# Optimization experiments

Hardware: AMD Instinct MI355X
Metric: run time of the kernel (lower is better)

Reference implementation:

```python
import jax, jax.numpy as jnp
import numpy as np

TOP_K = 2

def setup_inputs() -> dict:
    key = jax.random.key(0)
    k0, k1, k2, k3, k4 = jax.random.split(key, 5)
    B, S, D, H, E = 2, 2048, 1024, 2048, 8
    x = jax.random.normal(k0, (B, S, D), dtype=jnp.float32)
    router_w = jax.random.normal(k1, (D, E), dtype=jnp.float32) * (1.0 / np.sqrt(D))
    wg = jax.random.normal(k2, (E, D, H), dtype=jnp.float32) * (1.0 / np.sqrt(D))
    wu = jax.random.normal(k3, (E, D, H), dtype=jnp.float32) * (1.0 / np.sqrt(D))
    wd = jax.random.normal(k4, (E, H, D), dtype=jnp.float32) * (1.0 / np.sqrt(H))
    return {"x": x, "router_w": router_w, "wg": wg, "wu": wu, "wd": wd}

def reference(x, router_w, wg, wu, wd):
    B, S, D = x.shape
    E = router_w.shape[1]
    xf = x.reshape(-1, D)                                   # [T, D]
    router_logits = xf @ router_w                           # [T, E]
    top_logits, top_idx = jax.lax.top_k(router_logits, TOP_K)
    top_w = jax.nn.softmax(top_logits, axis=-1)             # [T, k]
    # Dense combine weights: W[t, e] = routing weight if e in top-k of t, else 0.
    combine = jnp.sum(jax.nn.one_hot(top_idx, E, dtype=x.dtype) * top_w[..., None], axis=1)  # [T, E]
    # SwiGLU experts, computed for all tokens and masked by the combine weights
    # (mathematically identical to the gather/scatter form in the original).
    gate = jnp.einsum('td,edh->eth', xf, wg)                # [E, T, H]
    up = jnp.einsum('td,edh->eth', xf, wu)                  # [E, T, H]
    fused = jax.nn.silu(gate) * up                          # [E, T, H]
    expert_out = jnp.einsum('eth,ehd->etd', fused, wd)      # [E, T, D]
    y = jnp.einsum('etd,te->td', expert_out, combine)       # [T, D]
    return y.reshape(B, S, D)
```

## Files before the change

kernel.cpp:

```cpp
#include <hip/hip_runtime.h>
#include <hip/hip_bf16.h>

#define T_TOK 4096
#define DDIM  1024
#define HDIM  2048
#define NEXP  8
#define BK 64

typedef __attribute__((ext_vector_type(4))) float f32x4;
typedef __attribute__((ext_vector_type(8))) short s16x8;
typedef __hip_bfloat16 bf16;

typedef const void __attribute__((address_space(1))) gvoid;
typedef void __attribute__((address_space(3))) svoid;

__device__ __forceinline__ void gload16(const void* g, void* l) {
    __builtin_amdgcn_global_load_lds((gvoid*)g, (svoid*)l, 16, 0, 0);
}

__global__ void router_kernel(const float* __restrict__ x, const float* __restrict__ rw,
                              int* __restrict__ r_e, float* __restrict__ r_w) {
    int wave = threadIdx.x >> 6, lane = threadIdx.x & 63;
    int t = blockIdx.x * 4 + wave;
    if (t >= T_TOK) return;
    const float* xr = x + (size_t)t * DDIM;
    double acc[NEXP];
#pragma unroll
    for (int e = 0; e < NEXP; ++e) acc[e] = 0.0;
    for (int d = lane; d < DDIM; d += 64) {
        float xv = xr[d];
        const float* rwr = rw + (size_t)d * NEXP;
#pragma unroll
        for (int e = 0; e < NEXP; ++e) acc[e] += (double)xv * (double)rwr[e];
    }
#pragma unroll
    for (int e = 0; e < NEXP; ++e) {
#pragma unroll
        for (int off = 32; off > 0; off >>= 1) acc[e] += __shfl_down(acc[e], off);
    }
    if (lane == 0) {
        int i0 = 0; double v0 = acc[0];
#pragma unroll
        for (int e = 1; e < NEXP; ++e) if (acc[e] > v0) { v0 = acc[e]; i0 = e; }
        int i1 = -1; double v1 = -1e300;
#pragma unroll
        for (int e = 0; e < NEXP; ++e) { if (e == i0) continue; if (acc[e] > v1) { v1 = acc[e]; i1 = e; } }
        float w0 = 1.0f / (1.0f + expf((float)(v1 - v0)));
        float w1 = 1.0f - w0;
        r_e[2*t]   = i0; r_e[2*t+1] = i1;
        r_w[2*t]   = w0; r_w[2*t+1] = w1;
    }
}

__global__ void count_kernel(const int* __restrict__ r_e, int* __restrict__ cnt) {
    int i = blockIdx.x * blockDim.x + threadIdx.x;
    if (i < 2 * T_TOK) atomicAdd(&cnt[r_e[i]], 1);
}
__global__ void scan_kernel(const int* __restrict__ cnt, int* __restrict__ offs) {
    if (threadIdx.x == 0) {
        int s = 0;
        for (int e = 0; e < NEXP; ++e) { offs[e] = s; s += cnt[e]; }
        offs[NEXP] = s;
    }
}
__global__ void fill_kernel(const int* __restrict__ r_e, const int* __restrict__ offs,
                            int* __restrict__ cnt2, const float* __restrict__ r_w,
                            int* __restrict__ list, float* __restrict__ slot_w) {
    int i = blockIdx.x * blockDim.x + threadIdx.x;
    if (i < 2 * T_TOK) {
        int e = r_e[i];
        int pos = atomicAdd(&cnt2[e], 1);
        int slot = offs[e] + pos;
        list[slot] = i >> 1;
        slot_w[slot] = r_w[i];
    }
}

__global__ void transpose_cast_kernel(const float* __restrict__ in, bf16* __restrict__ out,
                                      int R, int C, int rmul, int roff, size_t outE) {
    __shared__ bf16 tile[64][68];
    const float* inp = in + (size_t)blockIdx.z * R * C;
    bf16* outp = out + (size_t)blockIdx.z * outE;
    int r0 = blockIdx.x * 64, c0 = blockIdx.y * 64;
    int tid = threadIdx.x;
#pragma unroll
    for (int i = 0; i < 4; ++i) {
        int idx = i * 256 + tid;
        int r = idx >> 4, c4 = (idx & 15) * 4;
        float4 v = *reinterpret_cast<const float4*>(inp + (size_t)(r0 + r) * C + c0 + c4);
        tile[r][c4 + 0] = __float2bfloat16(v.x);
        tile[r][c4 + 1] = __float2bfloat16(v.y);
        tile[r][c4 + 2] = __float2bfloat16(v.z);
        tile[r][c4 + 3] = __float2bfloat16(v.w);
    }
    __syncthreads();
#pragma unroll
    for (int i = 0; i < 4; ++i) {
        int idx = i * 256 + tid;
        int c = idx >> 4, r4 = (idx & 15) * 4;
        union { ushort4 u; bf16 h[4]; } w;
        w.h[0] = tile[r4 + 0][c];
        w.h[1] = tile[r4 + 1][c];
        w.h[2] = tile[r4 + 2][c];
        w.h[3] = tile[r4 + 3][c];
        *reinterpret_cast<ushort4*>(outp + ((size_t)(c0 + c) * rmul + roff) * R + r0 + r4) = w.u;
    }
}

__global__ void cast_x_kernel(const float* __restrict__ x, bf16* __restrict__ xb) {
    size_t i = (size_t)(blockIdx.x * blockDim.x + threadIdx.x) * 4;
    float4 v = *reinterpret_cast<const float4*>(x + i);
    union { ushort4 u; bf16 h[4]; } o;
    o.h[0] = __float2bfloat16(v.x);
    o.h[1] = __float2bfloat16(v.y);
    o.h[2] = __float2bfloat16(v.z);
    o.h[3] = __float2bfloat16(v.w);
    *reinterpret_cast<ushort4*>(xb + i) = o.u;
}

__global__ __launch_bounds__(512, 4)
void gateup_kernel(const bf16* __restrict__ xb, const bf16* __restrict__ wguT,
                   const int* __restrict__ offs, const int* __restrict__ list,
                   bf16* __restrict__ hbuf) {
    int e = blockIdx.z;
    int base = offs[e];
    int ne = offs[e + 1] - base;
    int m0 = blockIdx.y * 128;
    if (m0 >= ne) return;
    int n0 = blockIdx.x * 128;

    __shared__ bf16 As[2][128 * 64];
    __shared__ bf16 Bs[2][128 * 64];

    int tid = threadIdx.x, lane = tid & 63, wid = tid >> 6;
    int sub = lane >> 3;
    int swz = 8 * ((lane & 7) ^ sub);

    const bf16* bbase = wguT + (size_t)e * (2 * HDIM) * DDIM + (size_t)n0 * DDIM;

    const bf16* aS[2]; const bf16* bS[2];
#pragma unroll
    for (int i = 0; i < 2; ++i) {
        int row = i * 64 + wid * 8 + sub;
        int r = m0 + row; if (r > ne - 1) r = ne - 1;
        aS[i] = xb + (size_t)list[base + r] * DDIM + swz;
        bS[i] = bbase + (size_t)row * DDIM + swz;
    }
    int dst0 = (wid * 8) * 64, dst1 = (64 + wid * 8) * 64;

    int wrow = (wid >> 2) * 64;
    int wcol = (wid & 3) * 32;
    int rl = lane & 15, kq = 8 * (lane >> 4);
    int xorv = (rl & 7) * 8;

    f32x4 zero4 = {0.f, 0.f, 0.f, 0.f};
    f32x4 acc[4][2];
#pragma unroll
    for (int mi = 0; mi < 4; ++mi) { acc[mi][0] = zero4; acc[mi][1] = zero4; }

    const int nk = DDIM / BK;

    gload16(aS[0], &As[0][dst0]);
    gload16(aS[1], &As[0][dst1]);
    gload16(bS[0], &Bs[0][dst0]);
    gload16(bS[1], &Bs[0][dst1]);
    gload16(aS[0] + BK, &As[1][dst0]);
    gload16(aS[1] + BK, &As[1][dst1]);
    gload16(bS[0] + BK, &Bs[1][dst0]);
    gload16(bS[1] + BK, &Bs[1][dst1]);

#define GU_COMPUTE(Ab, Bb)                                                        \
    _Pragma("unroll")                                                             \
    for (int kk = 0; kk < 2; ++kk) {                                              \
        int kos = (kk * 32 + kq) ^ xorv;                                          \
        s16x8 a[4], b[2];                                                         \
        _Pragma("unroll")                                                         \
        for (int mi = 0; mi < 4; ++mi)                                            \
            a[mi] = *reinterpret_cast<const s16x8*>(&(Ab)[(wrow + mi * 16 + rl) * 64 + kos]); \
        _Pragma("unroll")                                                         \
        for (int ni = 0; ni < 2; ++ni)                                            \
            b[ni] = *reinterpret_cast<const s16x8*>(&(Bb)[(wcol + ni * 16 + rl) * 64 + kos]); \
        _Pragma("unroll")                                                         \
        for (int mi = 0; mi < 4; ++mi)                                            \
            _Pragma("unroll")                                                     \
            for (int ni = 0; ni < 2; ++ni)                                        \
                acc[mi][ni] = __builtin_amdgcn_mfma_f32_16x16x32_bf16(a[mi], b[ni], acc[mi][ni], 0, 0, 0); \
    }

    for (int t = 0; t < nk - 1; ++t) {
        asm volatile("s_waitcnt vmcnt(4)" ::: "memory");
        __builtin_amdgcn_s_barrier();
        GU_COMPUTE(As[t & 1], Bs[t & 1]);
        __builtin_amdgcn_sched_barrier(0);
        __builtin_amdgcn_s_barrier();
        if (t + 2 < nk) {
            int k0 = (t + 2) * BK;
            gload16(aS[0] + k0, &As[t & 1][dst0]);
            gload16(aS[1] + k0, &As[t & 1][dst1]);
            gload16(bS[0] + k0, &Bs[t & 1][dst0]);
            gload16(bS[1] + k0, &Bs[t & 1][dst1]);
        }
    }
    asm volatile("s_waitcnt vmcnt(0)" ::: "memory");
    __builtin_amdgcn_s_barrier();
    GU_COMPUTE(As[(nk - 1) & 1], Bs[(nk - 1) & 1]);
#undef GU_COMPUTE

    int rbase = (lane >> 4) * 4, cbase = lane & 15;
    bool evenlane = (lane & 1) == 0;
#pragma unroll
    for (int mi = 0; mi < 4; ++mi) {
#pragma unroll
        for (int ni = 0; ni < 2; ++ni) {
#pragma unroll
            for (int r = 0; r < 4; ++r) {
                float own = acc[mi][ni][r];
                float oth = __shfl_xor(own, 1);
                int row = m0 + wrow + mi * 16 + rbase + r;
                if (evenlane && row < ne) {
                    float g = own, u = oth;
                    float h = (g / (1.0f + expf(-g))) * u;
                    int hcol = (n0 + wcol + ni * 16 + cbase) >> 1;
                    hbuf[(size_t)(base + row) * HDIM + hcol] = __float2bfloat16(h);
                }
            }
        }
    }
}

__global__ __launch_bounds__(512, 4)
void down_kernel(const bf16* __restrict__ hbuf, const bf16* __restrict__ wdT,
                 const int* __restrict__ offs, const int* __restrict__ list,
                 const float* __restrict__ slot_w, float* __restrict__ y) {
    int e = blockIdx.z;
    int base = offs[e];
    int ne = offs[e + 1] - base;
    int m0 = blockIdx.y * 128;
    if (m0 >= ne) return;
    int n0 = blockIdx.x * 128;

    __shared__ bf16 As[2][128 * 64];
    __shared__ bf16 Bs[2][128 * 64];

    int tid = threadIdx.x, lane = tid & 63, wid = tid >> 6;
    int sub = lane >> 3;
    int swz = 8 * ((lane & 7) ^ sub);

    const bf16* bbase = wdT + (size_t)e * DDIM * HDIM + (size_t)n0 * HDIM;

    const bf16* aS[2]; const bf16* bS[2];
#pragma unroll
    for (int i = 0; i < 2; ++i) {
        int row = i * 64 + wid * 8 + sub;
        int r = m0 + row; if (r > ne - 1) r = ne - 1;
        aS[i] = hbuf + (size_t)(base + r) * HDIM + swz;
        bS[i] = bbase + (size_t)row * HDIM + swz;
    }
    int dst0 = (wid * 8) * 64, dst1 = (64 + wid * 8) * 64;

    int wrow = (wid >> 2) * 64;
    int wcol = (wid & 3) * 32;
    int rl = lane & 15, kq = 8 * (lane >> 4);
    int xorv = (rl & 7) * 8;

    f32x4 zero4 = {0.f, 0.f, 0.f, 0.f};
    f32x4 acc[4][2];
#pragma unroll
    for (int mi = 0; mi < 4; ++mi) { acc[mi][0] = zero4; acc[mi][1] = zero4; }

    const int nk = HDIM / BK;

    gload16(aS[0], &As[0][dst0]);
    gload16(aS[1], &As[0][dst1]);
    gload16(bS[0], &Bs[0][dst0]);
    gload16(bS[1], &Bs[0][dst1]);
    gload16(aS[0] + BK, &As[1][dst0]);
    gload16(aS[1] + BK, &As[1][dst1]);
    gload16(bS[0] + BK, &Bs[1][dst0]);
    gload16(bS[1] + BK, &Bs[1][dst1]);

#define DN_COMPUTE(Ab, Bb)                                                        \
    _Pragma("unroll")                                                             \
    for (int kk = 0; kk < 2; ++kk) {                                              \
        int kos = (kk * 32 + kq) ^ xorv;                                          \
        s16x8 a[4], b[2];                                                         \
        _Pragma("unroll")                                                         \
        for (int mi = 0; mi < 4; ++mi)                                            \
            a[mi] = *reinterpret_cast<const s16x8*>(&(Ab)[(wrow + mi * 16 + rl) * 64 + kos]); \
        _Pragma("unroll")                                                         \
        for (int ni = 0; ni < 2; ++ni)                                            \
            b[ni] = *reinterpret_cast<const s16x8*>(&(Bb)[(wcol + ni * 16 + rl) * 64 + kos]); \
        _Pragma("unroll")                                                         \
        for (int mi = 0; mi < 4; ++mi)                                            \
            _Pragma("unroll")                                                     \
            for (int ni = 0; ni < 2; ++ni)                                        \
                acc[mi][ni] = __builtin_amdgcn_mfma_f32_16x16x32_bf16(a[mi], b[ni], acc[mi][ni], 0, 0, 0); \
    }

    for (int t = 0; t < nk - 1; ++t) {
        asm volatile("s_waitcnt vmcnt(4)" ::: "memory");
        __builtin_amdgcn_s_barrier();
        DN_COMPUTE(As[t & 1], Bs[t & 1]);
        __builtin_amdgcn_sched_barrier(0);
        __builtin_amdgcn_s_barrier();
        if (t + 2 < nk) {
            int k0 = (t + 2) * BK;
            gload16(aS[0] + k0, &As[t & 1][dst0]);
            gload16(aS[1] + k0, &As[t & 1][dst1]);
            gload16(bS[0] + k0, &Bs[t & 1][dst0]);
            gload16(bS[1] + k0, &Bs[t & 1][dst1]);
        }
    }
    asm volatile("s_waitcnt vmcnt(0)" ::: "memory");
    __builtin_amdgcn_s_barrier();
    DN_COMPUTE(As[(nk - 1) & 1], Bs[(nk - 1) & 1]);
#undef DN_COMPUTE

    int rbase = (lane >> 4) * 4, cbase = lane & 15;
#pragma unroll
    for (int mi = 0; mi < 4; ++mi) {
#pragma unroll
        for (int r = 0; r < 4; ++r) {
            int row = m0 + wrow + mi * 16 + rbase + r;
            if (row < ne) {
                int slot = base + row;
                int tok = list[slot];
                float w = slot_w[slot];
                float* yrow = y + (size_t)tok * DDIM + n0 + wcol + cbase;
#pragma unroll
                for (int ni = 0; ni < 2; ++ni)
                    atomicAdd(yrow + ni * 16, w * acc[mi][ni][r]);
            }
        }
    }
}

extern "C" void kernel_launch(void* const* d_in, const int* in_sizes, int n_in,
                              void* d_out, int out_size, void* d_ws, size_t ws_size,
                              hipStream_t stream) {
    const float* x  = (const float*)d_in[0];
    const float* rw = (const float*)d_in[1];
    const float* wg = (const float*)d_in[2];
    const float* wu = (const float*)d_in[3];
    const float* wd = (const float*)d_in[4];
    float* y = (float*)d_out;

    char* ws = (char*)d_ws;
    int*   r_e    = (int*)  (ws + 0);
    float* r_w    = (float*)(ws + 32768);
    int*   cnt    = (int*)  (ws + 65536);
    int*   cnt2   = (int*)  (ws + 65568);
    int*   offs   = (int*)  (ws + 65600);
    int*   list   = (int*)  (ws + 65664);
    float* slot_w = (float*)(ws + 98432);
    bf16*  xb     = (bf16*) (ws + 1048576ull);
    bf16*  wguT   = (bf16*) (ws + 16777216ull);
    bf16*  wdT    = (bf16*) (ws + 83886080ull);
    bf16*  hbuf   = (bf16*) (ws + 117440512ull);

    transpose_cast_kernel<<<dim3(DDIM / 64, HDIM / 64, NEXP), 256, 0, stream>>>(
        wg, wguT, DDIM, HDIM, 2, 0, (size_t)2 * HDIM * DDIM);
    transpose_cast_kernel<<<dim3(DDIM / 64, HDIM / 64, NEXP), 256, 0, stream>>>(
        wu, wguT, DDIM, HDIM, 2, 1, (size_t)2 * HDIM * DDIM);
    transpose_cast_kernel<<<dim3(HDIM / 64, DDIM / 64, NEXP), 256, 0, stream>>>(
        wd, wdT, HDIM, DDIM, 1, 0, (size_t)DDIM * HDIM);
    cast_x_kernel<<<dim3(T_TOK * DDIM / 4 / 256), 256, 0, stream>>>(x, xb);

    router_kernel<<<dim3(T_TOK / 4), 256, 0, stream>>>(x, rw, r_e, r_w);
    hipMemsetAsync(ws + 65536, 0, 64, stream);
    count_kernel<<<dim3(2 * T_TOK / 256), 256, 0, stream>>>(r_e, cnt);
    scan_kernel<<<dim3(1), 64, 0, stream>>>(cnt, offs);
    fill_kernel<<<dim3(2 * T_TOK / 256), 256, 0, stream>>>(r_e, offs, cnt2, r_w, list, slot_w);

    hipMemsetAsync(d_out, 0, (size_t)out_size * sizeof(float), stream);

    gateup_kernel<<<dim3(2 * HDIM / 128, T_TOK / 128, NEXP), 512, 0, stream>>>(xb, wguT, offs, list, hbuf);
    down_kernel<<<dim3(DDIM / 128, T_TOK / 128, NEXP), 512, 0, stream>>>(hbuf, wdT, offs, list, slot_w, y);
}
```

Measured before the change: 329.9 us.

## Enlarge MoE GEMM block tiles with dynamic LDS and MFMA priority hints

Gate-up GEMM tiles grow from 128x128 to 256x256 (each wave computes 128x64), and the down GEMM tile grows to 128x256, with shared memory moved to dynamic allocations of 128KB and 96KB. Each k-step is split into two phases with an extra barrier, and s_setprio is raised around the MFMA bursts. The goal is more reuse per LDS load, less global traffic per FLOP and fewer atomics per output. In exchange there are more registers per thread, lower occupancy (launch bounds drop to 2), fewer blocks, and more tail waste on experts with few tokens.

```diff
diff --git a/kernel.cpp b/kernel.cpp
--- a/kernel.cpp
+++ b/kernel.cpp
@@ -118,19 +118,20 @@
     *reinterpret_cast<ushort4*>(xb + i) = o.u;
 }
 
-__global__ __launch_bounds__(512, 4)
+__global__ __launch_bounds__(512, 2)
 void gateup_kernel(const bf16* __restrict__ xb, const bf16* __restrict__ wguT,
                    const int* __restrict__ offs, const int* __restrict__ list,
                    bf16* __restrict__ hbuf) {
     int e = blockIdx.z;
     int base = offs[e];
     int ne = offs[e + 1] - base;
-    int m0 = blockIdx.y * 128;
+    int m0 = blockIdx.y * 256;
     if (m0 >= ne) return;
-    int n0 = blockIdx.x * 128;
-
-    __shared__ bf16 As[2][128 * 64];
-    __shared__ bf16 Bs[2][128 * 64];
+    int n0 = blockIdx.x * 256;
+
+    extern __shared__ __align__(16) char smem[];
+    bf16* As = (bf16*)smem;
+    bf16* Bs = (bf16*)(smem + 65536);
 
     int tid = threadIdx.x, lane = tid & 63, wid = tid >> 6;
     int sub = lane >> 3;
@@ -138,80 +139,96 @@
 
     const bf16* bbase = wguT + (size_t)e * (2 * HDIM) * DDIM + (size_t)n0 * DDIM;
 
-    const bf16* aS[2]; const bf16* bS[2];
-#pragma unroll
-    for (int i = 0; i < 2; ++i) {
+    const bf16* aS[4]; const bf16* bS[4];
+    int dstA[4], dstB[4];
+#pragma unroll
+    for (int i = 0; i < 4; ++i) {
         int row = i * 64 + wid * 8 + sub;
         int r = m0 + row; if (r > ne - 1) r = ne - 1;
         aS[i] = xb + (size_t)list[base + r] * DDIM + swz;
         bS[i] = bbase + (size_t)row * DDIM + swz;
-    }
-    int dst0 = (wid * 8) * 64, dst1 = (64 + wid * 8) * 64;
-
-    int wrow = (wid >> 2) * 64;
-    int wcol = (wid & 3) * 32;
+        dstA[i] = (i * 64 + wid * 8) * 64;
+        dstB[i] = dstA[i];
+    }
+
+    int wrow = (wid >> 2) * 128;
+    int wcol = (wid & 3) * 64;
     int rl = lane & 15, kq = 8 * (lane >> 4);
     int xorv = (rl & 7) * 8;
 
     f32x4 zero4 = {0.f, 0.f, 0.f, 0.f};
-    f32x4 acc[4][2];
-#pragma unroll
-    for (int mi = 0; mi < 4; ++mi) { acc[mi][0] = zero4; acc[mi][1] = zero4; }
+    f32x4 acc[8][4];
+#pragma unroll
+    for (int mi = 0; mi < 8; ++mi)
+#pragma unroll
+        for (int ni = 0; ni < 4; ++ni) acc[mi][ni] = zero4;
 
     const int nk = DDIM / BK;
 
-    gload16(aS[0], &As[0][dst0]);
-    gload16(aS[1], &As[0][dst1]);
-    gload16(bS[0], &Bs[0][dst0]);
-    gload16(bS[1], &Bs[0][dst1]);
-    gload16(aS[0] + BK, &As[1][dst0]);
-    gload16(aS[1] + BK, &As[1][dst1]);
-    gload16(bS[0] + BK, &Bs[1][dst0]);
-    gload16(bS[1] + BK, &Bs[1][dst1]);
-
-#define GU_COMPUTE(Ab, Bb)                                                        \
-    _Pragma("unroll")                                                             \
-    for (int kk = 0; kk < 2; ++kk) {                                              \
-        int kos = (kk * 32 + kq) ^ xorv;                                          \
-        s16x8 a[4], b[2];                                                         \
-        _Pragma("unroll")                                                         \
-        for (int mi = 0; mi < 4; ++mi)                                            \
+#pragma unroll
+    for (int i = 0; i < 4; ++i) { gload16(aS[i], As + dstA[i]); }
+#pragma unroll
+    for (int i = 0; i < 4; ++i) { gload16(bS[i], Bs + dstB[i]); }
+#pragma unroll
+    for (int i = 0; i < 4; ++i) { gload16(aS[i] + BK, As + 16384 + dstA[i]); }
+#pragma unroll
+    for (int i = 0; i < 4; ++i) { gload16(bS[i] + BK, Bs + 16384 + dstB[i]); }
+
+#define GU_PHASE(Ab, Bb, kk)                                                             \
+    {                                                                                    \
+        int kos = ((kk) * 32 + kq) ^ xorv;                                               \
+        s16x8 a[8], b[4];                                                                \
+        _Pragma("unroll")                                                                \
+        for (int mi = 0; mi < 8; ++mi)                                                   \
             a[mi] = *reinterpret_cast<const s16x8*>(&(Ab)[(wrow + mi * 16 + rl) * 64 + kos]); \
-        _Pragma("unroll")                                                         \
-        for (int ni = 0; ni < 2; ++ni)                                            \
+        _Pragma("unroll")                                                                \
+        for (int ni = 0; ni < 4; ++ni)                                                   \
             b[ni] = *reinterpret_cast<const s16x8*>(&(Bb)[(wcol + ni * 16 + rl) * 64 + kos]); \
-        _Pragma("unroll")                                                         \
-        for (int mi = 0; mi < 4; ++mi)                                            \
-            _Pragma("unroll")                                                     \
-            for (int ni = 0; ni < 2; ++ni)                                        \
+        __builtin_amdgcn_s_setprio(1);                                                   \
+        _Pragma("unroll")                                                                \
+        for (int mi = 0; mi < 8; ++mi)                                                   \
+            _Pragma("unroll")                                                            \
+            for (int ni = 0; ni < 4; ++ni)                                               \
                 acc[mi][ni] = __builtin_amdgcn_mfma_f32_16x16x32_bf16(a[mi], b[ni], acc[mi][ni], 0, 0, 0); \
+        __builtin_amdgcn_s_setprio(0);                                                   \
     }
 
     for (int t = 0; t < nk - 1; ++t) {
-        asm volatile("s_waitcnt vmcnt(4)" ::: "memory");
-        __builtin_amdgcn_s_barrier();
-        GU_COMPUTE(As[t & 1], Bs[t & 1]);
+        asm volatile("s_waitcnt vmcnt(8)" ::: "memory");
+        __builtin_amdgcn_s_barrier();
+        const bf16* Ab = As + (t & 1) * 16384;
+        const bf16* Bb = Bs + (t & 1) * 16384;
+        GU_PHASE(Ab, Bb, 0);
+        __builtin_amdgcn_s_barrier();
+        GU_PHASE(Ab, Bb, 1);
         __builtin_amdgcn_sched_barrier(0);
         __builtin_amdgcn_s_barrier();
         if (t + 2 < nk) {
             int k0 = (t + 2) * BK;
-            gload16(aS[0] + k0, &As[t & 1][dst0]);
-            gload16(aS[1] + k0, &As[t & 1][dst1]);
-            gload16(bS[0] + k0, &Bs[t & 1][dst0]);
-            gload16(bS[1] + k0, &Bs[t & 1][dst1]);
+            bf16* Ad = As + (t & 1) * 16384;
+            bf16* Bd = Bs + (t & 1) * 16384;
+#pragma unroll
+            for (int i = 0; i < 4; ++i) { gload16(aS[i] + k0, Ad + dstA[i]); }
+#pragma unroll
+            for (int i = 0; i < 4; ++i) { gload16(bS[i] + k0, Bd + dstB[i]); }
         }
     }
     asm volatile("s_waitcnt vmcnt(0)" ::: "memory");
     __builtin_amdgcn_s_barrier();
-    GU_COMPUTE(As[(nk - 1) & 1], Bs[(nk - 1) & 1]);
-#undef GU_COMPUTE
+    {
+        const bf16* Ab = As + ((nk - 1) & 1) * 16384;
+        const bf16* Bb = Bs + ((nk - 1) & 1) * 16384;
+        GU_PHASE(Ab, Bb, 0);
+        GU_PHASE(Ab, Bb, 1);
+    }
+#undef GU_PHASE
 
     int rbase = (lane >> 4) * 4, cbase = lane & 15;
     bool evenlane = (lane & 1) == 0;
 #pragma unroll
-    for (int mi = 0; mi < 4; ++mi) {
-#pragma unroll
-        for (int ni = 0; ni < 2; ++ni) {
+    for (int mi = 0; mi < 8; ++mi) {
+#pragma unroll
+        for (int ni = 0; ni < 4; ++ni) {
 #pragma unroll
             for (int r = 0; r < 4; ++r) {
                 float own = acc[mi][ni][r];
@@ -228,7 +245,7 @@
     }
 }
 
-__global__ __launch_bounds__(512, 4)
+__global__ __launch_bounds__(512, 2)
 void down_kernel(const bf16* __restrict__ hbuf, const bf16* __restrict__ wdT,
                  const int* __restrict__ offs, const int* __restrict__ list,
                  const float* __restrict__ slot_w, float* __restrict__ y) {
@@ -237,10 +254,11 @@
     int ne = offs[e + 1] - base;
     int m0 = blockIdx.y * 128;
     if (m0 >= ne) return;
-    int n0 = blockIdx.x * 128;
-
-    __shared__ bf16 As[2][128 * 64];
-    __shared__ bf16 Bs[2][128 * 64];
+    int n0 = blockIdx.x * 256;
+
+    extern __shared__ __align__(16) char smem[];
+    bf16* As = (bf16*)smem;
+    bf16* Bs = (bf16*)(smem + 32768);
 
     int tid = threadIdx.x, lane = tid & 63, wid = tid >> 6;
     int sub = lane >> 3;
@@ -248,73 +266,93 @@
 
     const bf16* bbase = wdT + (size_t)e * DDIM * HDIM + (size_t)n0 * HDIM;
 
-    const bf16* aS[2]; const bf16* bS[2];
+    const bf16* aS[2]; const bf16* bS[4];
+    int dstA[2], dstB[4];
 #pragma unroll
     for (int i = 0; i < 2; ++i) {
         int row = i * 64 + wid * 8 + sub;
         int r = m0 + row; if (r > ne - 1) r = ne - 1;
         aS[i] = hbuf + (size_t)(base + r) * HDIM + swz;
+        dstA[i] = (i * 64 + wid * 8) * 64;
+    }
+#pragma unroll
+    for (int i = 0; i < 4; ++i) {
+        int row = i * 64 + wid * 8 + sub;
         bS[i] = bbase + (size_t)row * HDIM + swz;
-    }
-    int dst0 = (wid * 8) * 64, dst1 = (64 + wid * 8) * 64;
+        dstB[i] = (i * 64 + wid * 8) * 64;
+    }
 
     int wrow = (wid >> 2) * 64;
-    int wcol = (wid & 3) * 32;
+    int wcol = (wid & 3) * 64;
     int rl = lane & 15, kq = 8 * (lane >> 4);
     int xorv = (rl & 7) * 8;
 
     f32x4 zero4 = {0.f, 0.f, 0.f, 0.f};
-    f32x4 acc[4][2];
-#pragma unroll
-    for (int mi = 0; mi < 4; ++mi) { acc[mi][0] = zero4; acc[mi][1] = zero4; }
+    f32x4 acc[4][4];
+#pragma unroll
+    for (int mi = 0; mi < 4; ++mi)
+#pragma unroll
+        for (int ni = 0; ni < 4; ++ni) acc[mi][ni] = zero4;
 
     const int nk = HDIM / BK;
 
-    gload16(aS[0], &As[0][dst0]);
-    gload16(aS[1], &As[0][dst1]);
-    gload16(bS[0], &Bs[0][dst0]);
-    gload16(bS[1], &Bs[0][dst1]);
-    gload16(aS[0] + BK, &As[1][dst0]);
-    gload16(aS[1] + BK, &As[1][dst1]);
-    gload16(bS[0] + BK, &Bs[1][dst0]);
-    gload16(bS[1] + BK, &Bs[1][dst1]);
-
-#define DN_COMPUTE(Ab, Bb)                                                        \
-    _Pragma("unroll")                                                             \
-    for (int kk = 0; kk < 2; ++kk) {                                              \
-        int kos = (kk * 32 + kq) ^ xorv;                                          \
-        s16x8 a[4], b[2];                                                         \
-        _Pragma("unroll")                                                         \
-        for (int mi = 0; mi < 4; ++mi)                                            \
+#pragma unroll
+    for (int i = 0; i < 2; ++i) { gload16(aS[i], As + dstA[i]); }
+#pragma unroll
+    for (int i = 0; i < 4; ++i) { gload16(bS[i], Bs + dstB[i]); }
+#pragma unroll
+    for (int i = 0; i < 2; ++i) { gload16(aS[i] + BK, As + 8192 + dstA[i]); }
+#pragma unroll
+    for (int i = 0; i < 4; ++i) { gload16(bS[i] + BK, Bs + 16384 + dstB[i]); }
+
+#define DN_PHASE(Ab, Bb, kk)                                                             \
+    {                                                                                    \
+        int kos = ((kk) * 32 + kq) ^ xorv;                                               \
+        s16x8 a[4], b[4];                                                                \
+        _Pragma("unroll")                                                                \
+        for (int mi = 0; mi < 4; ++mi)                                                   \
             a[mi] = *reinterpret_cast<const s16x8*>(&(Ab)[(wrow + mi * 16 + rl) * 64 + kos]); \
-        _Pragma("unroll")                                                         \
-        for (int ni = 0; ni < 2; ++ni)                                            \
+        _Pragma("unroll")                                                                \
+        for (int ni = 0; ni < 4; ++ni)                                                   \
             b[ni] = *reinterpret_cast<const s16x8*>(&(Bb)[(wcol + ni * 16 + rl) * 64 + kos]); \
-        _Pragma("unroll")                                                         \
-        for (int mi = 0; mi < 4; ++mi)                                            \
-            _Pragma("unroll")                                                     \
-            for (int ni = 0; ni < 2; ++ni)                                        \
+        __builtin_amdgcn_s_setprio(1);                                                   \
+        _Pragma("unroll")                                                                \
+        for (int mi = 0; mi < 4; ++mi)                                                   \
+            _Pragma("unroll")                                                            \
+            for (int ni = 0; ni < 4; ++ni)                                               \
                 acc[mi][ni] = __builtin_amdgcn_mfma_f32_16x16x32_bf16(a[mi], b[ni], acc[mi][ni], 0, 0, 0); \
+        __builtin_amdgcn_s_setprio(0);                                                   \
     }
 
     for (int t = 0; t < nk - 1; ++t) {
-        asm volatile("s_waitcnt vmcnt(4)" ::: "memory");
-        __builtin_amdgcn_s_barrier();
-        DN_COMPUTE(As[t & 1], Bs[t & 1]);
+        asm volatile("s_waitcnt vmcnt(6)" ::: "memory");
+        __builtin_amdgcn_s_barrier();
+        const bf16* Ab = As + (t & 1) * 8192;
+        const bf16* Bb = Bs + (t & 1) * 16384;
+        DN_PHASE(Ab, Bb, 0);
+        __builtin_amdgcn_s_barrier();
+        DN_PHASE(Ab, Bb, 1);
         __builtin_amdgcn_sched_barrier(0);
         __builtin_amdgcn_s_barrier();
         if (t + 2 < nk) {
             int k0 = (t + 2) * BK;
-            gload16(aS[0] + k0, &As[t & 1][dst0]);
-            gload16(aS[1] + k0, &As[t & 1][dst1]);
-            gload16(bS[0] + k0, &Bs[t & 1][dst0]);
-            gload16(bS[1] + k0, &Bs[t & 1][dst1]);
+            bf16* Ad = As + (t & 1) * 8192;
+            bf16* Bd = Bs + (t & 1) * 16384;
+#pragma unroll
+            for (int i = 0; i < 2; ++i) { gload16(aS[i] + k0, Ad + dstA[i]); }
+#pragma unroll
+            for (int i = 0; i < 4; ++i) { gload16(bS[i] + k0, Bd + dstB[i]); }
         }
     }
     asm volatile("s_waitcnt vmcnt(0)" ::: "memory");
     __builtin_amdgcn_s_barrier();
-    DN_COMPUTE(As[(nk - 1) & 1], Bs[(nk - 1) & 1]);
-#undef DN_COMPUTE
+    {
+        const bf16* Ab = As + ((nk - 1) & 1) * 8192;
+        const bf16* Bb = Bs + ((nk - 1) & 1) * 16384;
+        DN_PHASE(Ab, Bb, 0);
+        DN_PHASE(Ab, Bb, 1);
+    }
+#undef DN_PHASE
 
     int rbase = (lane >> 4) * 4, cbase = lane & 15;
 #pragma unroll
@@ -328,7 +366,7 @@
                 float w = slot_w[slot];
                 float* yrow = y + (size_t)tok * DDIM + n0 + wcol + cbase;
 #pragma unroll
-                for (int ni = 0; ni < 2; ++ni)
+                for (int ni = 0; ni < 4; ++ni)
                     atomicAdd(yrow + ni * 16, w * acc[mi][ni][r]);
             }
         }
@@ -344,6 +382,9 @@
     const float* wu = (const float*)d_in[3];
     const float* wd = (const float*)d_in[4];
     float* y = (float*)d_out;
+
+    hipFuncSetAttribute((const void*)gateup_kernel, hipFuncAttributeMaxDynamicSharedMemorySize, 131072);
+    hipFuncSetAttribute((const void*)down_kernel,   hipFuncAttributeMaxDynamicSharedMemorySize, 98304);
 
     char* ws = (char*)d_ws;
     int*   r_e    = (int*)  (ws + 0);
@@ -374,6 +415,6 @@
 
     hipMemsetAsync(d_out, 0, (size_t)out_size * sizeof(float), stream);
 
-    gateup_kernel<<<dim3(2 * HDIM / 128, T_TOK / 128, NEXP), 512, 0, stream>>>(xb, wguT, offs, list, hbuf);
-    down_kernel<<<dim3(DDIM / 128, T_TOK / 128, NEXP), 512, 0, stream>>>(hbuf, wdT, offs, list, slot_w, y);
-}
+    gateup_kernel<<<dim3(2 * HDIM / 256, T_TOK / 256, NEXP), 512, 131072, stream>>>(xb, wguT, offs, list, hbuf);
+    down_kernel<<<dim3(DDIM / 256, T_TOK / 128, NEXP), 512, 98304, stream>>>(hbuf, wdT, offs, list, slot_w, y);
+}
```

Measured after the change: 370.1 us. 12.2% more time.
